# Optimization experiments

Measured on AMD Instinct MI355X. Metric: run time of the kernel, lower is better.

Reference implementation:

```python
import jax, jax.numpy as jnp
import numpy as np

B, T, N_EMBD, HEAD_SIZE = 8, 2048, 1024, 128

def setup_inputs() -> dict:
    key = jax.random.key(0)
    kx, kk, kq, kv = jax.random.split(key, 4)
    scale = 1.0 / np.sqrt(N_EMBD)
    return {
        "x": jax.random.normal(kx, (B, T, N_EMBD), dtype=jnp.float32),
        "Wk": jax.random.normal(kk, (N_EMBD, HEAD_SIZE), dtype=jnp.float32) * scale,
        "Wq": jax.random.normal(kq, (N_EMBD, HEAD_SIZE), dtype=jnp.float32) * scale,
        "Wv": jax.random.normal(kv, (N_EMBD, HEAD_SIZE), dtype=jnp.float32) * scale,
    }

def reference(x, Wk, Wq, Wv):
    # x: [B, T, C]; projections: [C, H]
    k = jnp.einsum("btc,ch->bth", x, Wk)
    q = jnp.einsum("btc,ch->bth", x, Wq)
    v = jnp.einsum("btc,ch->bth", x, Wv)
    # NOTE: original code does tf.divide(scores, 1/sqrt(n_embd)) == scores * sqrt(n_embd)
    wei = jnp.einsum("bqh,bkh->bqk", q, k) * jnp.sqrt(jnp.float32(N_EMBD))  # [B, T, T]
    # causal mask via band_part (zero out upper triangle) then zeros -> -inf, as in source
    tril = jnp.tril(wei)
    wei = jnp.where(tril == 0.0, -jnp.inf, tril)
    wei = jax.nn.softmax(wei, axis=-1)
    out = jnp.einsum("bqk,bkh->bqh", wei, v)  # [B, T, H]
    return out
```

## Files before the change

kernel.cpp:

```cpp
#include <hip/hip_runtime.h>
#include <hip/hip_bf16.h>

typedef float  f32x4  __attribute__((ext_vector_type(4)));
typedef __bf16 bf16x8 __attribute__((ext_vector_type(8)));
typedef unsigned int   u32;
typedef unsigned short u16;
typedef u32   u32x2  __attribute__((ext_vector_type(2)));
typedef u32   u32x4  __attribute__((ext_vector_type(4)));
typedef u16   u16x4  __attribute__((ext_vector_type(4)));
typedef u16   u16x8  __attribute__((ext_vector_type(8)));

#define DEV __device__ __forceinline__

constexpr int NB = 8, T = 2048, C = 1024, H = 128;
constexpr int BT = NB * T;

union Frag {
  bf16x8 v;
  u32x4  u4;
  u32x2  u2[2];
  u32    u[4];
  u16    s[8];
};

DEV u16 f2bu(float f) {
  __hip_bfloat16 h = __float2bfloat16(f);
  return __builtin_bit_cast(u16, h);
}
DEV float bu2f(u16 u) {
  return __bfloat162float(__builtin_bit_cast(__hip_bfloat16, u));
}
DEV f32x4 MFMA(bf16x8 a, bf16x8 b, f32x4 c) {
  return __builtin_amdgcn_mfma_f32_16x16x32_bf16(a, b, c, 0, 0, 0);
}


__global__ void prep_w(const float* __restrict__ Wk, const float* __restrict__ Wq,
                       const float* __restrict__ Wv,
                       u16* __restrict__ wpq, u16* __restrict__ wpk,
                       u16* __restrict__ wpv) {
  const int id = blockIdx.x * 256 + threadIdx.x;
  if (id >= 24 * 32 * 64) return;
  const int lane = id & 63;
  const int kc   = (id >> 6) & 31;
  const int tile = id >> 11;
  const int mat  = tile >> 3;
  const int tt   = tile & 7;
  const int n    = tt * 16 + (lane & 15);
  const float* W = (mat == 0) ? Wq : (mat == 1) ? Wk : Wv;
  u16x8 hi, lo;
  #pragma unroll
  for (int e = 0; e < 8; ++e) {
    const int k = kc * 32 + 4 * (lane >> 4) + (e & 3) + 16 * (e >> 2);
    const float w = W[(size_t)k * H + n];
    u16 h = f2bu(w);
    hi[e] = h;
    lo[e] = f2bu(w - bu2f(h));
  }
  if (mat == 2) {
    *(u16x8*)(wpv + ((size_t)(tt * 32 + kc) * 64 + lane) * 8) = hi;
  } else {
    u16* p = ((mat == 0) ? wpq : wpk) +
             (((size_t)(tt * 32 + kc) * 2 + 0) * 64 + lane) * 8;
    *(u16x8*)p         = hi;
    *(u16x8*)(p + 512) = lo;
  }
}

__global__ __launch_bounds__(256, 2) void proj_kernel(
    const float* __restrict__ x,
    const u16* __restrict__ wpq, const u16* __restrict__ wpk,
    const u16* __restrict__ wpv,
    u16* __restrict__ qpk, u16* __restrict__ kpk, u16* __restrict__ vpk) {
  __shared__ u16 xh[2][64][72];
  __shared__ u16 xl[2][64][72];
  __shared__ u16 wsl[2][1280 * 8];
  const int tid  = threadIdx.x;
  const int ng   = blockIdx.x >> 8;
  const int mt   = blockIdx.x & 255;
  const int m0   = mt * 64;
  const int w    = tid >> 6;
  const int lane = tid & 63;
  const int lg   = lane >> 4, lc = lane & 15;

  const int lrow = tid >> 2;
  const int lcs  = (tid & 3) * 16;

  const float* xsrc = x + (size_t)(m0 + lrow) * C + lcs;
  const u16* wbase[5];
  int wstep[5];
  #pragma unroll
  for (int i = 0; i < 5; ++i) {
    const int c = tid + 256 * i;
    const int kcg   = c >= 640;
    const int rem   = c - kcg * 640;
    const int plane = rem >> 6;
    const int ln    = rem & 63;
    const u16* base;
    int stride;
    if (plane < 4) {
      base = wpq + (size_t)((2 * ng + (plane >> 1)) * 32) * 1024 +
             (plane & 1) * 512 + ln * 8;
      stride = 1024;
    } else if (plane < 8) {
      const int p = plane - 4;
      base = wpk + (size_t)((2 * ng + (p >> 1)) * 32) * 1024 +
             (p & 1) * 512 + ln * 8;
      stride = 1024;
    } else {
      base = wpv + (size_t)((2 * ng + (plane - 8)) * 32) * 512 + ln * 8;
      stride = 512;
    }
    wbase[i] = base + kcg * stride;
    wstep[i] = 2 * stride;
  }

  f32x4 zero = {0.f, 0.f, 0.f, 0.f};
  f32x4 acc[6];
  #pragma unroll
  for (int j = 0; j < 6; ++j) acc[j] = zero;

  f32x4 xv[4];
  u16x8 wreg[5];

  auto stage_load = [&](int ks) {
    #pragma unroll
    for (int j = 0; j < 4; ++j)
      xv[j] = *(const f32x4*)(xsrc + ks * 64 + 4 * j);
    #pragma unroll
    for (int i = 0; i < 5; ++i)
      wreg[i] = *(const u16x8*)(wbase[i] + (size_t)ks * wstep[i]);
  };

  auto stage_write = [&](int buf) {
    #pragma unroll
    for (int j = 0; j < 4; ++j) {
      u16x4 hv, lv;
      #pragma unroll
      for (int e = 0; e < 4; ++e) {
        u16 h = f2bu(xv[j][e]);
        hv[e] = h;
        lv[e] = f2bu(xv[j][e] - bu2f(h));
      }
      *(u16x4*)&xh[buf][lrow][lcs + 4 * j] = hv;
      *(u16x4*)&xl[buf][lrow][lcs + 4 * j] = lv;
    }
    #pragma unroll
    for (int i = 0; i < 5; ++i)
      *(u16x8*)&wsl[buf][(size_t)(tid + 256 * i) * 8] = wreg[i];
  };

  auto compute = [&](int buf) {
    #pragma unroll
    for (int kc = 0; kc < 2; ++kc) {
      Frag axh, axl;
      const int row = 16 * w + lc;
      axh.u2[0] = *(const u32x2*)&xh[buf][row][kc * 32 + 4 * lg];
      axh.u2[1] = *(const u32x2*)&xh[buf][row][kc * 32 + 16 + 4 * lg];
      axl.u2[0] = *(const u32x2*)&xl[buf][row][kc * 32 + 4 * lg];
      axl.u2[1] = *(const u32x2*)&xl[buf][row][kc * 32 + 16 + 4 * lg];
      #pragma unroll
      for (int jt = 0; jt < 2; ++jt) {
        {
          Frag bh, bl;
          bh.u4 = *(const u32x4*)&wsl[buf][((size_t)(kc * 10 + jt * 2 + 0) * 64 + lane) * 8];
          bl.u4 = *(const u32x4*)&wsl[buf][((size_t)(kc * 10 + jt * 2 + 1) * 64 + lane) * 8];
          acc[jt] = MFMA(axh.v, bh.v, acc[jt]);
          acc[jt] = MFMA(axh.v, bl.v, acc[jt]);
          acc[jt] = MFMA(axl.v, bh.v, acc[jt]);
        }
        {
          Frag bh, bl;
          bh.u4 = *(const u32x4*)&wsl[buf][((size_t)(kc * 10 + 4 + jt * 2 + 0) * 64 + lane) * 8];
          bl.u4 = *(const u32x4*)&wsl[buf][((size_t)(kc * 10 + 4 + jt * 2 + 1) * 64 + lane) * 8];
          acc[2 + jt] = MFMA(axh.v, bh.v, acc[2 + jt]);
          acc[2 + jt] = MFMA(axh.v, bl.v, acc[2 + jt]);
          acc[2 + jt] = MFMA(axl.v, bh.v, acc[2 + jt]);
        }
        {
          Frag bh;
          bh.u4 = *(const u32x4*)&wsl[buf][((size_t)(kc * 10 + 8 + jt) * 64 + lane) * 8];
          acc[4 + jt] = MFMA(axh.v, bh.v, acc[4 + jt]);
        }
      }
    }
  };

  stage_load(0);
  stage_write(0);
  __syncthreads();
  int cur = 0;
  for (int ks = 0; ks < 16; ++ks) {
    if (ks < 15) stage_load(ks + 1);
    compute(cur);
    if (ks < 15) stage_write(cur ^ 1);
    __syncthreads();
    cur ^= 1;
  }

  const int tb_abs = mt * 4 + w;
  const int b  = tb_abs >> 7;
  const int tb = tb_abs & 127;
  #pragma unroll
  for (int j = 0; j < 6; ++j) {
    const int mat = j >> 1;
    const int jt  = j & 1;
    const int tt  = 2 * ng + jt;
    #pragma unroll
    for (int r = 0; r < 4; ++r) {
      const float val = acc[j][r];
      if (mat < 2) {
        const u16 hvv = f2bu(val);
        const u16 lvv = f2bu(val - bu2f(hvv));
        const int lane_c = 4 * lg + r + 16 * (lc >> 2);
        const int hs = tt >> 1;
        const int e  = (lc & 3) + 4 * (tt & 1);
        u16* dst = ((mat == 0) ? qpk : kpk) +
                   (((size_t)(b * 128 + tb) * 4 + hs) * 2 * 64 + lane_c) * 8 + e;
        dst[0]   = hvv;
        dst[512] = lvv;
      } else {
        const int kt = tb >> 1;
        const int lane_c = lc + 16 * lg;
        const int e = r + 4 * (tb & 1);
        vpk[(((size_t)(b * 64 + kt) * 8 + tt) * 64 + lane_c) * 8 + e] = f2bu(val);
      }
    }
  }
}

__global__ __launch_bounds__(512, 4) void attn_kernel(
    const u16* __restrict__ qpk, const u16* __restrict__ kpk,
    const u16* __restrict__ vpk, float* __restrict__ out) {
  __shared__ float lm[8][16];
  __shared__ float ll[8][16];
  __shared__ u16 lo[8][16][132];

  const int bid = blockIdx.x;
  const int b   = bid & 7;
  const int qt  = bid >> 3;
  const int w    = threadIdx.x >> 6;
  const int lane = threadIdx.x & 63;
  const int lg = lane >> 4, lc = lane & 15;

  Frag bqh[4], bql[4];
  const u16* qp = qpk + (size_t)(b * 128 + qt) * 4096 + lane * 8;
  #pragma unroll
  for (int hs = 0; hs < 4; ++hs) {
    bqh[hs].u4 = *(const u32x4*)(qp + (size_t)(hs * 2 + 0) * 512);
    bql[hs].u4 = *(const u32x4*)(qp + (size_t)(hs * 2 + 1) * 512);
  }

  f32x4 zero = {0.f, 0.f, 0.f, 0.f};
  f32x4 o_acc[8];
  #pragma unroll
  for (int i = 0; i < 8; ++i) o_acc[i] = zero;
  float m_run = -INFINITY, l_run = 0.f;

  const int myq = qt * 16 + lc;
  const int nkb = qt >> 2;

  for (int kb = w; kb <= nkb; kb += 8) {
    f32x4 s[4];
    #pragma unroll
    for (int t = 0; t < 4; ++t) s[t] = zero;

    const u16* kp = kpk + (size_t)(b * 128 + kb * 4) * 4096 + lane * 8;
    __builtin_amdgcn_s_setprio(1);
    #pragma unroll
    for (int t = 0; t < 4; ++t) {
      #pragma unroll
      for (int hs = 0; hs < 4; ++hs) {
        const u16* p = kp + (size_t)(t * 8 + hs * 2) * 512;
        Frag akh, akl;
        akh.u4 = *(const u32x4*)p;
        akl.u4 = *(const u32x4*)(p + 512);
        s[t] = MFMA(akh.v, bqh[hs].v, s[t]);
        s[t] = MFMA(akh.v, bql[hs].v, s[t]);
        s[t] = MFMA(akl.v, bqh[hs].v, s[t]);
      }
    }
    __builtin_amdgcn_s_setprio(0);

    float pmax = -INFINITY;
    #pragma unroll
    for (int t = 0; t < 4; ++t) {
      #pragma unroll
      for (int r = 0; r < 4; ++r) {
        const int kk = kb * 64 + t * 16 + 4 * lg + r;
        float v = s[t][r] * 32.0f;
        if (kk > myq || v == 0.0f) v = -INFINITY;
        s[t][r] = v;
        pmax = fmaxf(pmax, v);
      }
    }
    pmax = fmaxf(pmax, __shfl_xor(pmax, 16));
    pmax = fmaxf(pmax, __shfl_xor(pmax, 32));
    const float m_new = fmaxf(m_run, pmax);
    const float alpha = __expf(m_run - m_new);

    float sum = 0.f;
    u16 pb[16];
    #pragma unroll
    for (int t = 0; t < 4; ++t) {
      #pragma unroll
      for (int r = 0; r < 4; ++r) {
        const float p = __expf(s[t][r] - m_new);
        sum += p;
        pb[t * 4 + r] = f2bu(p);
      }
    }
    sum += __shfl_xor(sum, 16);
    sum += __shfl_xor(sum, 32);
    l_run = l_run * alpha + sum;
    m_run = m_new;

    float al[4];
    #pragma unroll
    for (int r = 0; r < 4; ++r) al[r] = __shfl(alpha, 4 * lg + r);
    #pragma unroll
    for (int i = 0; i < 8; ++i) {
      #pragma unroll
      for (int r = 0; r < 4; ++r) o_acc[i][r] *= al[r];
    }

    Frag pa[2];
    #pragma unroll
    for (int ks = 0; ks < 2; ++ks) {
      #pragma unroll
      for (int e = 0; e < 8; ++e)
        pa[ks].s[e] = pb[(2 * ks + (e >> 2)) * 4 + (e & 3)];
    }

    __builtin_amdgcn_s_setprio(1);
    #pragma unroll
    for (int ks = 0; ks < 2; ++ks) {
      const u16* vp = vpk + (size_t)(b * 64 + kb * 2 + ks) * 4096 + lane * 8;
      #pragma unroll
      for (int ht = 0; ht < 8; ++ht) {
        Frag bv;
        bv.u4 = *(const u32x4*)(vp + (size_t)ht * 512);
        o_acc[ht] = MFMA(pa[ks].v, bv.v, o_acc[ht]);
      }
    }
    __builtin_amdgcn_s_setprio(0);
  }

  if (lane < 16) { lm[w][lane] = m_run; ll[w][lane] = l_run; }
  #pragma unroll
  for (int ht = 0; ht < 8; ++ht)
    #pragma unroll
    for (int r = 0; r < 4; ++r)
      lo[w][4 * lg + r][ht * 16 + lc] = f2bu(o_acc[ht][r]);
  __syncthreads();

  const int tid = threadIdx.x;
  const int q  = tid >> 5;
  const int hb = (tid & 31) * 4;
  float M = -INFINITY;
  #pragma unroll
  for (int ww = 0; ww < 8; ++ww) M = fmaxf(M, lm[ww][q]);
  float lsum = 0.f;
  f32x4 osum = {0.f, 0.f, 0.f, 0.f};
  #pragma unroll
  for (int ww = 0; ww < 8; ++ww) {
    const float sc = __expf(lm[ww][q] - M);
    lsum += sc * ll[ww][q];
    const u16x4 ov = *(const u16x4*)&lo[ww][q][hb];
    #pragma unroll
    for (int j = 0; j < 4; ++j) osum[j] += sc * bu2f(ov[j]);
  }
  const float inv = 1.0f / lsum;
  f32x4 res = {osum[0] * inv, osum[1] * inv, osum[2] * inv, osum[3] * inv};
  *(f32x4*)&out[((size_t)(b * T + qt * 16 + q)) * H + hb] = res;
}

extern "C" void kernel_launch(void* const* d_in, const int* in_sizes, int n_in,
                              void* d_out, int out_size, void* d_ws, size_t ws_size,
                              hipStream_t stream) {
  (void)in_sizes; (void)n_in; (void)out_size; (void)ws_size;
  const float* x  = (const float*)d_in[0];
  const float* Wk = (const float*)d_in[1];
  const float* Wq = (const float*)d_in[2];
  const float* Wv = (const float*)d_in[3];
  float* out = (float*)d_out;

  u16* w = (u16*)d_ws;
  const size_t WPQK = (size_t)8 * 32 * 2 * 64 * 8;
  const size_t WPV  = (size_t)8 * 32 * 64 * 8;
  const size_t QKP  = (size_t)NB * 128 * 4 * 2 * 64 * 8;
  u16* wpq = w;
  u16* wpk = wpq + WPQK;
  u16* wpv = wpk + WPQK;
  u16* qpk = wpv + WPV;
  u16* kpk = qpk + QKP;
  u16* vpk = kpk + QKP;

  prep_w<<<192, 256, 0, stream>>>(Wk, Wq, Wv, wpq, wpk, wpv);
  proj_kernel<<<1024, 256, 0, stream>>>(x, wpq, wpk, wpv, qpk, kpk, vpk);
  attn_kernel<<<NB * (T / 16), 512, 0, stream>>>(qpk, kpk, vpk, out);
}
```

Measured before the change: 103.3 us.

## Retile projection kernel: load x directly into registers, drop x LDS staging

The projection kernel now covers 128 rows and one 16-wide output column group per block instead of 64 rows and two column groups. Each wave reads its x rows straight from global memory into registers and splits them into bf16 hi/lo there, so the LDS tiles and bf16 split for x are gone. Weight staging is prefetched two steps ahead, and the occupancy hint rises to 4 blocks per SM. This removes LDS traffic and a barrier's worth of work for x, but every weight slice is now read by more blocks, and the x global loads sit in the compute loop with little latency hiding.

```diff
diff --git a/kernel.cpp b/kernel.cpp
--- a/kernel.cpp
+++ b/kernel.cpp
@@ -67,26 +67,20 @@
   }
 }
 
-__global__ __launch_bounds__(256, 2) void proj_kernel(
+__global__ __launch_bounds__(256, 4) void proj_kernel(
     const float* __restrict__ x,
     const u16* __restrict__ wpq, const u16* __restrict__ wpk,
     const u16* __restrict__ wpv,
     u16* __restrict__ qpk, u16* __restrict__ kpk, u16* __restrict__ vpk) {
-  __shared__ u16 xh[2][64][72];
-  __shared__ u16 xl[2][64][72];
   __shared__ u16 wsl[2][1280 * 8];
   const int tid  = threadIdx.x;
-  const int ng   = blockIdx.x >> 8;
-  const int mt   = blockIdx.x & 255;
-  const int m0   = mt * 64;
+  const int ng   = blockIdx.x >> 7;
+  const int mt   = blockIdx.x & 127;
+  const int m0   = mt * 128;
   const int w    = tid >> 6;
   const int lane = tid & 63;
   const int lg   = lane >> 4, lc = lane & 15;
 
-  const int lrow = tid >> 2;
-  const int lcs  = (tid & 3) * 16;
-
-  const float* xsrc = x + (size_t)(m0 + lrow) * C + lcs;
   const u16* wbase[5];
   int wstep[5];
   #pragma unroll
@@ -98,132 +92,118 @@
     const int ln    = rem & 63;
     const u16* base;
     int stride;
-    if (plane < 4) {
-      base = wpq + (size_t)((2 * ng + (plane >> 1)) * 32) * 1024 +
-             (plane & 1) * 512 + ln * 8;
+    if (plane < 2) {
+      base = wpq + (size_t)(ng * 32) * 1024 + plane * 512 + ln * 8;
       stride = 1024;
-    } else if (plane < 8) {
-      const int p = plane - 4;
-      base = wpk + (size_t)((2 * ng + (p >> 1)) * 32) * 1024 +
-             (p & 1) * 512 + ln * 8;
+    } else if (plane < 4) {
+      base = wpk + (size_t)(ng * 32) * 1024 + (plane - 2) * 512 + ln * 8;
       stride = 1024;
     } else {
-      base = wpv + (size_t)((2 * ng + (plane - 8)) * 32) * 512 + ln * 8;
+      base = wpv + (size_t)(ng * 32) * 512 + ln * 8;
       stride = 512;
     }
     wbase[i] = base + kcg * stride;
     wstep[i] = 2 * stride;
   }
 
+  const float* xs0 = x + (size_t)(m0 + 32 * w + lc) * C + 4 * lg;
+  const float* xs1 = xs0 + 16 * C;
+
   f32x4 zero = {0.f, 0.f, 0.f, 0.f};
-  f32x4 acc[6];
-  #pragma unroll
-  for (int j = 0; j < 6; ++j) acc[j] = zero;
-
-  f32x4 xv[4];
+  f32x4 accq[2], acck[2], accv[2];
+  #pragma unroll
+  for (int s = 0; s < 2; ++s) { accq[s] = zero; acck[s] = zero; accv[s] = zero; }
+
   u16x8 wreg[5];
-
-  auto stage_load = [&](int ks) {
-    #pragma unroll
-    for (int j = 0; j < 4; ++j)
-      xv[j] = *(const f32x4*)(xsrc + ks * 64 + 4 * j);
+  auto loadW = [&](int ks) {
+    const int k = ks > 15 ? 15 : ks;
     #pragma unroll
     for (int i = 0; i < 5; ++i)
-      wreg[i] = *(const u16x8*)(wbase[i] + (size_t)ks * wstep[i]);
+      wreg[i] = *(const u16x8*)(wbase[i] + (size_t)k * wstep[i]);
   };
-
-  auto stage_write = [&](int buf) {
-    #pragma unroll
-    for (int j = 0; j < 4; ++j) {
-      u16x4 hv, lv;
-      #pragma unroll
-      for (int e = 0; e < 4; ++e) {
-        u16 h = f2bu(xv[j][e]);
-        hv[e] = h;
-        lv[e] = f2bu(xv[j][e] - bu2f(h));
-      }
-      *(u16x4*)&xh[buf][lrow][lcs + 4 * j] = hv;
-      *(u16x4*)&xl[buf][lrow][lcs + 4 * j] = lv;
-    }
+  auto writeW = [&](int buf) {
     #pragma unroll
     for (int i = 0; i < 5; ++i)
       *(u16x8*)&wsl[buf][(size_t)(tid + 256 * i) * 8] = wreg[i];
   };
 
-  auto compute = [&](int buf) {
+  auto compute = [&](int buf, int ks) {
+    f32x4 xr0[4], xr1[4];
+    #pragma unroll
+    for (int j = 0; j < 4; ++j) {
+      xr0[j] = *(const f32x4*)(xs0 + ks * 64 + 16 * j);
+      xr1[j] = *(const f32x4*)(xs1 + ks * 64 + 16 * j);
+    }
     #pragma unroll
     for (int kc = 0; kc < 2; ++kc) {
-      Frag axh, axl;
-      const int row = 16 * w + lc;
-      axh.u2[0] = *(const u32x2*)&xh[buf][row][kc * 32 + 4 * lg];
-      axh.u2[1] = *(const u32x2*)&xh[buf][row][kc * 32 + 16 + 4 * lg];
-      axl.u2[0] = *(const u32x2*)&xl[buf][row][kc * 32 + 4 * lg];
-      axl.u2[1] = *(const u32x2*)&xl[buf][row][kc * 32 + 16 + 4 * lg];
-      #pragma unroll
-      for (int jt = 0; jt < 2; ++jt) {
-        {
-          Frag bh, bl;
-          bh.u4 = *(const u32x4*)&wsl[buf][((size_t)(kc * 10 + jt * 2 + 0) * 64 + lane) * 8];
-          bl.u4 = *(const u32x4*)&wsl[buf][((size_t)(kc * 10 + jt * 2 + 1) * 64 + lane) * 8];
-          acc[jt] = MFMA(axh.v, bh.v, acc[jt]);
-          acc[jt] = MFMA(axh.v, bl.v, acc[jt]);
-          acc[jt] = MFMA(axl.v, bh.v, acc[jt]);
-        }
-        {
-          Frag bh, bl;
-          bh.u4 = *(const u32x4*)&wsl[buf][((size_t)(kc * 10 + 4 + jt * 2 + 0) * 64 + lane) * 8];
-          bl.u4 = *(const u32x4*)&wsl[buf][((size_t)(kc * 10 + 4 + jt * 2 + 1) * 64 + lane) * 8];
-          acc[2 + jt] = MFMA(axh.v, bh.v, acc[2 + jt]);
-          acc[2 + jt] = MFMA(axh.v, bl.v, acc[2 + jt]);
-          acc[2 + jt] = MFMA(axl.v, bh.v, acc[2 + jt]);
-        }
-        {
-          Frag bh;
-          bh.u4 = *(const u32x4*)&wsl[buf][((size_t)(kc * 10 + 8 + jt) * 64 + lane) * 8];
-          acc[4 + jt] = MFMA(axh.v, bh.v, acc[4 + jt]);
-        }
-      }
+      Frag axh0, axl0, axh1, axl1;
+      #pragma unroll
+      for (int e = 0; e < 4; ++e) {
+        u16 h;
+        h = f2bu(xr0[2 * kc][e]);     axh0.s[e] = h;     axl0.s[e] = f2bu(xr0[2 * kc][e] - bu2f(h));
+        h = f2bu(xr0[2 * kc + 1][e]); axh0.s[e + 4] = h; axl0.s[e + 4] = f2bu(xr0[2 * kc + 1][e] - bu2f(h));
+        h = f2bu(xr1[2 * kc][e]);     axh1.s[e] = h;     axl1.s[e] = f2bu(xr1[2 * kc][e] - bu2f(h));
+        h = f2bu(xr1[2 * kc + 1][e]); axh1.s[e + 4] = h; axl1.s[e + 4] = f2bu(xr1[2 * kc + 1][e] - bu2f(h));
+      }
+      const u16* wb = &wsl[buf][(size_t)(kc * 640) * 8];
+      Frag qh, ql, kh, kl, vh;
+      qh.u4 = *(const u32x4*)(wb + ((size_t)(0 * 64) + lane) * 8);
+      ql.u4 = *(const u32x4*)(wb + ((size_t)(1 * 64) + lane) * 8);
+      kh.u4 = *(const u32x4*)(wb + ((size_t)(2 * 64) + lane) * 8);
+      kl.u4 = *(const u32x4*)(wb + ((size_t)(3 * 64) + lane) * 8);
+      vh.u4 = *(const u32x4*)(wb + ((size_t)(4 * 64) + lane) * 8);
+      accq[0] = MFMA(axh0.v, qh.v, accq[0]);  accq[1] = MFMA(axh1.v, qh.v, accq[1]);
+      accq[0] = MFMA(axh0.v, ql.v, accq[0]);  accq[1] = MFMA(axh1.v, ql.v, accq[1]);
+      accq[0] = MFMA(axl0.v, qh.v, accq[0]);  accq[1] = MFMA(axl1.v, qh.v, accq[1]);
+      acck[0] = MFMA(axh0.v, kh.v, acck[0]);  acck[1] = MFMA(axh1.v, kh.v, acck[1]);
+      acck[0] = MFMA(axh0.v, kl.v, acck[0]);  acck[1] = MFMA(axh1.v, kl.v, acck[1]);
+      acck[0] = MFMA(axl0.v, kh.v, acck[0]);  acck[1] = MFMA(axl1.v, kh.v, acck[1]);
+      accv[0] = MFMA(axh0.v, vh.v, accv[0]);  accv[1] = MFMA(axh1.v, vh.v, accv[1]);
     }
   };
 
-  stage_load(0);
-  stage_write(0);
+  loadW(0);
+  writeW(0);
+  loadW(1);
   __syncthreads();
   int cur = 0;
   for (int ks = 0; ks < 16; ++ks) {
-    if (ks < 15) stage_load(ks + 1);
-    compute(cur);
-    if (ks < 15) stage_write(cur ^ 1);
+    writeW(cur ^ 1);
+    loadW(ks + 2);
+    compute(cur, ks);
     __syncthreads();
     cur ^= 1;
   }
 
-  const int tb_abs = mt * 4 + w;
-  const int b  = tb_abs >> 7;
-  const int tb = tb_abs & 127;
-  #pragma unroll
-  for (int j = 0; j < 6; ++j) {
-    const int mat = j >> 1;
-    const int jt  = j & 1;
-    const int tt  = 2 * ng + jt;
+  #pragma unroll
+  for (int s = 0; s < 2; ++s) {
+    const int tb_abs = mt * 8 + 2 * w + s;
+    const int b  = tb_abs >> 7;
+    const int tb = tb_abs & 127;
+    const int hs = ng >> 1;
+    const int eq = (lc & 3) + 4 * (ng & 1);
+    const int lane_cq = 4 * lg + 16 * (lc >> 2);
     #pragma unroll
     for (int r = 0; r < 4; ++r) {
-      const float val = acc[j][r];
-      if (mat < 2) {
+      {
+        const float val = accq[s][r];
         const u16 hvv = f2bu(val);
-        const u16 lvv = f2bu(val - bu2f(hvv));
-        const int lane_c = 4 * lg + r + 16 * (lc >> 2);
-        const int hs = tt >> 1;
-        const int e  = (lc & 3) + 4 * (tt & 1);
-        u16* dst = ((mat == 0) ? qpk : kpk) +
-                   (((size_t)(b * 128 + tb) * 4 + hs) * 2 * 64 + lane_c) * 8 + e;
+        u16* dst = qpk + (((size_t)(b * 128 + tb) * 4 + hs) * 2 * 64 + lane_cq + r) * 8 + eq;
         dst[0]   = hvv;
-        dst[512] = lvv;
-      } else {
+        dst[512] = f2bu(val - bu2f(hvv));
+      }
+      {
+        const float val = acck[s][r];
+        const u16 hvv = f2bu(val);
+        u16* dst = kpk + (((size_t)(b * 128 + tb) * 4 + hs) * 2 * 64 + lane_cq + r) * 8 + eq;
+        dst[0]   = hvv;
+        dst[512] = f2bu(val - bu2f(hvv));
+      }
+      {
         const int kt = tb >> 1;
         const int lane_c = lc + 16 * lg;
         const int e = r + 4 * (tb & 1);
-        vpk[(((size_t)(b * 64 + kt) * 8 + tt) * 64 + lane_c) * 8 + e] = f2bu(val);
+        vpk[(((size_t)(b * 64 + kt) * 8 + ng) * 64 + lane_c) * 8 + e] = f2bu(accv[s][r]);
       }
     }
   }
```

New measurement: 133.4 us. 1.29x slower.
